# Performance work log

Measured on AMD Instinct MI355X. Metric: run time of the kernel, lower is better.

## Reference

```python
import jax, jax.numpy as jnp
import numpy as np

B, S, D, H = 2, 2048, 1024, 16
HD = D // H  # 64


def rotate_half(x):
    x1, x2 = x[..., : x.shape[-1] // 2], x[..., x.shape[-1] // 2 :]
    return jnp.concatenate((-x2, x1), axis=-1)


def setup_inputs() -> dict:
    key = jax.random.key(0)
    ks = jax.random.split(key, 8)
    return {
        "hidden_states": jax.random.normal(ks[0], (B, S, D), jnp.float32),
        "attention_bias": jax.random.normal(ks[1], (B, 1, S, S), jnp.float32),
        "cos": jax.random.uniform(ks[2], (1, S, 1, HD), jnp.float32),
        "sin": jax.random.uniform(ks[3], (1, S, 1, HD), jnp.float32),
        "Wqkv": jax.random.normal(ks[4], (D, 3 * D), jnp.float32) * (D ** -0.5),
        "bqkv": jnp.zeros((3 * D,), jnp.float32),
        "Wo": jax.random.normal(ks[5], (D, D), jnp.float32) * (D ** -0.5),
        "bo": jnp.zeros((D,), jnp.float32),
    }


def reference(hidden_states, attention_bias, cos, sin, Wqkv, bqkv, Wo, bo):
    # packed QKV projection: [B,S,D] -> [B,S,3D]
    qkv = hidden_states @ Wqkv + bqkv
    q, k, v = jnp.split(qkv, 3, axis=-1)
    # reshape to [B,S,H,HD]
    q = q.reshape(B, S, H, HD)
    k = k.reshape(B, S, H, HD)
    v = v.reshape(B, S, H, HD)
    # rotary position embedding
    q = q * cos + rotate_half(q) * sin
    k = k * cos + rotate_half(k) * sin
    # scaled dot-product attention with additive bias
    scores = jnp.einsum("bqhd,bkhd->bhqk", q, k) / jnp.sqrt(jnp.float32(HD))
    scores = scores + attention_bias
    probs = jax.nn.softmax(scores, axis=-1)
    ctx = jnp.einsum("bhqk,bkhd->bqhd", probs, v)  # [B,S,H,HD]
    ctx = ctx.reshape(B, S, D)
    return ctx @ Wo + bo
```

## Files before the change

kernel.cpp:

```cpp
#include <hip/hip_runtime.h>
#include <stdint.h>

typedef unsigned short u16;
typedef __attribute__((ext_vector_type(8))) short short8;
typedef __attribute__((ext_vector_type(4))) float f32x4;

#define DI __device__ __forceinline__

constexpr int S_LEN = 2048;
constexpr float LOG2E = 1.44269504088896f;
constexpr float SC = 0.125f * 1.44269504088896f;

DI float bf2f(u16 u) { union { uint32_t i; float f; } v; v.i = ((uint32_t)u) << 16; return v.f; }
DI u16 f2bf(float f) {
  union { float f; uint32_t i; } v; v.f = f;
  return (u16)((v.i + 0x7FFFu + ((v.i >> 16) & 1u)) >> 16);
}
DI uint32_t cvtpk(float lo, float hi) {
  uint32_t r;
  asm("v_cvt_pk_bf16_f32 %0, %1, %2" : "=v"(r) : "v"(lo), "v"(hi));
  return r;
}
DI float exp2r(float x) {
  float r;
  asm("v_exp_f32 %0, %1" : "=v"(r) : "v"(x));
  return r;
}

DI void cp16(const void* g, void* l) {
  auto gp = reinterpret_cast<const __attribute__((address_space(1))) uint32_t*>(
      reinterpret_cast<uintptr_t>(g));
  auto lp = reinterpret_cast<__attribute__((address_space(3))) uint32_t*>(
      reinterpret_cast<uintptr_t>(l));
  __builtin_amdgcn_global_load_lds(gp, lp, 16, 0, 0);
}

DI f32x4 mfma16(short8 a, short8 b, f32x4 c) {
  return __builtin_amdgcn_mfma_f32_16x16x32_bf16(a, b, c, 0, 0, 0);
}

DI int permk(int rl) {
  return ((rl >> 5) & 1) * 32 + ((rl >> 2) & 3) * 8 + ((rl >> 4) & 1) * 4 + (rl & 3);
}

__global__ __launch_bounds__(256) void k_cvt(const float* __restrict__ in,
                                             u16* __restrict__ out, int n4) {
  int i = blockIdx.x * 256 + threadIdx.x;
  if (i >= n4) return;
  float4 v = ((const float4*)in)[i];
  ushort4 o = { f2bf(v.x), f2bf(v.y), f2bf(v.z), f2bf(v.w) };
  ((ushort4*)out)[i] = o;
}

__global__ __launch_bounds__(256) void k_cvtb(const float* __restrict__ in,
                                              u16* __restrict__ out, int n4) {
  int i = blockIdx.x * 256 + threadIdx.x;
  if (i >= n4) return;
  float4 v = ((const float4*)in)[i];
  ushort4 o = { f2bf(v.x * LOG2E), f2bf(v.y * LOG2E), f2bf(v.z * LOG2E), f2bf(v.w * LOG2E) };
  ((ushort4*)out)[i] = o;
}

__global__ __launch_bounds__(256) void k_tr(const float* __restrict__ in,
                                            u16* __restrict__ out, int R, int C) {
  __shared__ float t[32][33];
  int tx = threadIdx.x & 31, ty = threadIdx.x >> 5;
  int c0 = blockIdx.x * 32, r0 = blockIdx.y * 32;
#pragma unroll
  for (int k = 0; k < 4; k++)
    t[ty + 8 * k][tx] = in[(size_t)(r0 + ty + 8 * k) * C + c0 + tx];
  __syncthreads();
#pragma unroll
  for (int k = 0; k < 4; k++)
    out[(size_t)(c0 + ty + 8 * k) * R + r0 + tx] = f2bf(t[tx][ty + 8 * k]);
}

template <int STORE_F32, int ROPE>
__global__ __launch_bounds__(256) void k_gemm(const u16* __restrict__ A,
                                              const u16* __restrict__ Bt,
                                              const float* __restrict__ bias,
                                              void* __restrict__ Cout,
                                              const float* __restrict__ cosb,
                                              const float* __restrict__ sinb,
                                              int N, int K, int nbx) {
  __shared__ u16 Al[128 * 32];
  __shared__ u16 Bl[128 * 32];
  int nwg = gridDim.x;
  int per = nwg >> 3;
  int id = blockIdx.x;
  int sid = (id & 7) * per + (id >> 3);
  int bx = sid % nbx, by = sid / nbx;
  int row0 = by * 128, col0 = bx * 128;
  int tid = threadIdx.x;
  int lane = tid & 63, wave = tid >> 6;
  int lg = lane >> 4, lc = lane & 15;
  int wr = wave >> 1, wc = wave & 1;
  int srow = tid >> 2, sseg = tid & 3;
  const u16* ga = A + (size_t)(row0 + srow) * K + sseg * 8;
  const u16* gb = Bt + (size_t)(col0 + srow) * K + sseg * 8;
  u16* la = Al + tid * 8;
  u16* lb = Bl + tid * 8;
  size_t half = (size_t)64 * K;
  f32x4 acc[4][4] = {};
  for (int ko = 0; ko < K; ko += 32) {
    cp16(ga + ko, la);
    cp16(ga + ko + half, la + 2048);
    cp16(gb + ko, lb);
    cp16(gb + ko + half, lb + 2048);
    __syncthreads();
    short8 af[4], bf[4];
#pragma unroll
    for (int i = 0; i < 4; i++)
      af[i] = *(const short8*)&Al[(wr * 64 + i * 16 + lc) * 32 + lg * 8];
#pragma unroll
    for (int j = 0; j < 4; j++)
      bf[j] = *(const short8*)&Bl[(wc * 64 + j * 16 + lc) * 32 + lg * 8];
#pragma unroll
    for (int i = 0; i < 4; i++)
#pragma unroll
      for (int j = 0; j < 4; j++) acc[i][j] = mfma16(af[i], bf[j], acc[i][j]);
    __syncthreads();
  }
  int cbase = col0 + wc * 64 + lc;
  float bv[4];
#pragma unroll
  for (int j = 0; j < 4; j++) bv[j] = bias[cbase + j * 16];
  bool do_rope = false;
  if constexpr (ROPE) do_rope = (col0 < 2048);
#pragma unroll
  for (int i = 0; i < 4; i++) {
    int r = row0 + wr * 64 + i * 16 + lg * 4;
#pragma unroll
    for (int q = 0; q < 4; q++) {
      float v[4];
#pragma unroll
      for (int j = 0; j < 4; j++) v[j] = acc[i][j][q] + bv[j];
      if (do_rope) {
        int s = (r + q) & 2047;
        const float* cb = cosb + s * 64 + lc;
        const float* sb = sinb + s * 64 + lc;
#pragma unroll
        for (int jp = 0; jp < 2; jp++) {
          float cl = cb[jp * 16], sl = sb[jp * 16];
          float ch = cb[jp * 16 + 32], sh = sb[jp * 16 + 32];
          float x1 = v[jp], x2 = v[jp + 2];
          v[jp] = x1 * cl - x2 * sl;
          v[jp + 2] = x2 * ch + x1 * sh;
        }
      }
#pragma unroll
      for (int j = 0; j < 4; j++) {
        if constexpr (STORE_F32)
          ((float*)Cout)[(size_t)(r + q) * N + cbase + j * 16] = v[j];
        else
          ((u16*)Cout)[(size_t)(r + q) * N + cbase + j * 16] = f2bf(v[j]);
      }
    }
  }
}

__global__ __launch_bounds__(256) void k_vtrans(const u16* __restrict__ qkv,
                                                u16* __restrict__ vtg) {
  __shared__ u16 Vl[64 * 66];
  int bh = blockIdx.y, b = bh >> 4, h = bh & 15;
  int s0 = blockIdx.x * 64;
  int tid = threadIdx.x;
  int r = tid >> 3, seg = tid & 7;
  const u16* src = qkv + (size_t)(b * S_LEN + s0) * 3072 + 2048 + h * 64 + seg * 8;
#pragma unroll
  for (int p = 0; p < 2; p++) {
    int s = r + 32 * p;
    short8 v = *(const short8*)(src + (size_t)s * 3072);
    const uint32_t* vw = (const uint32_t*)&v;
    uint32_t* dst = (uint32_t*)&Vl[s * 66 + seg * 8];
#pragma unroll
    for (int q = 0; q < 4; q++) dst[q] = vw[q];
  }
  __syncthreads();
  u16* out = vtg + (size_t)bh * 64 * 2048 + s0 + seg * 8;
#pragma unroll
  for (int p = 0; p < 2; p++) {
    int d = r + 32 * p;
    short8 o;
#pragma unroll
    for (int j = 0; j < 8; j++) o[j] = (short)Vl[(seg * 8 + j) * 66 + d];
    *(short8*)(out + (size_t)d * 2048) = o;
  }
}

DI float sm_pa(const f32x4 st[4], const short8* bc, short8 pa[2]) {
  float acc = 0.f;
  uint32_t w[4][2];
#pragma unroll
  for (int j = 0; j < 4; j++) {
    int base = (j & 1) * 4;
    float b0 = bf2f((u16)(j < 2 ? bc[0][base + 0] : bc[1][base + 0]));
    float b1 = bf2f((u16)(j < 2 ? bc[0][base + 1] : bc[1][base + 1]));
    float b2 = bf2f((u16)(j < 2 ? bc[0][base + 2] : bc[1][base + 2]));
    float b3 = bf2f((u16)(j < 2 ? bc[0][base + 3] : bc[1][base + 3]));
    float e0 = exp2r(st[j][0] * SC + b0);
    float e1 = exp2r(st[j][1] * SC + b1);
    float e2 = exp2r(st[j][2] * SC + b2);
    float e3 = exp2r(st[j][3] * SC + b3);
    acc += (e0 + e1) + (e2 + e3);
    w[j][0] = cvtpk(e0, e1);
    w[j][1] = cvtpk(e2, e3);
  }
  union { short8 s; uint32_t u[4]; } p0, p1;
  p0.u[0] = w[0][0]; p0.u[1] = w[0][1]; p0.u[2] = w[1][0]; p0.u[3] = w[1][1];
  p1.u[0] = w[2][0]; p1.u[1] = w[2][1]; p1.u[2] = w[3][0]; p1.u[3] = w[3][1];
  pa[0] = p0.s;
  pa[1] = p1.s;
  return acc;
}

DI void attn_store(u16* __restrict__ ctx, const f32x4 o[4], float lsumT,
                   size_t rowbase, int hcol, int lg, int lc) {
  float rinv[4];
#pragma unroll
  for (int r = 0; r < 4; r++) rinv[r] = 1.0f / __shfl(lsumT, lg * 4 + r);
#pragma unroll
  for (int j = 0; j < 4; j++)
#pragma unroll
    for (int r = 0; r < 4; r++)
      ctx[(rowbase + lg * 4 + r) * 1024 + hcol + j * 16 + lc] =
          f2bf(o[j][r] * rinv[r]);
}

__global__ __launch_bounds__(256, 2) void k_attn(const u16* __restrict__ qkv,
                                                 const u16* __restrict__ biasl2,
                                                 const u16* __restrict__ vtg,
                                                 u16* __restrict__ ctx) {
  __shared__ u16 Kl[2][4096];
  __shared__ u16 Vl[2][4096];
  constexpr int nkt = 32;
  int id = blockIdx.x;
  int idx = id >> 3;
  int bh = (id & 7) * 4 + (idx & 3);
  int qt = idx >> 2;
  int b = bh >> 4, h = bh & 15;
  int tid = threadIdx.x, lane = tid & 63, wave = tid >> 6;
  int lg = lane >> 4, lc = lane & 15;
  int q0 = qt * 128 + wave * 32;

  const u16* qb = qkv + (size_t)(b * S_LEN + q0 + lc) * 3072 + h * 64 + lg * 8;
  short8 qf[2][2];
#pragma unroll
  for (int s = 0; s < 2; s++) {
    qf[s][0] = *(const short8*)(qb + (size_t)s * 16 * 3072);
    qf[s][1] = *(const short8*)(qb + (size_t)s * 16 * 3072 + 32);
  }

  int srow = tid >> 3, sseg = tid & 7;
  const u16* kst[2];
  const u16* vst[2];
#pragma unroll
  for (int p = 0; p < 2; p++) {
    int rl = srow + 32 * p;
    int sw = (sseg ^ (rl & 7)) * 8;
    kst[p] = qkv + (size_t)(b * S_LEN + permk(rl)) * 3072 + 1024 + h * 64 + sw;
    vst[p] = vtg + (size_t)bh * 64 * 2048 + (size_t)rl * 2048 + sw;
  }

  const u16* bp0 = biasl2 + ((size_t)b * S_LEN + q0 + lc) * 2048 + lg * 8;
  const u16* bp1 = bp0 + (size_t)16 * 2048;

  f32x4 o0[4] = {}, o1[4] = {};
  float lsum0 = 0.f, lsum1 = 0.f;

#pragma unroll
  for (int p = 0; p < 2; p++) {
    cp16(kst[p], (u16*)&Kl[0][0] + p * 2048 + tid * 8);
    cp16(vst[p], (u16*)&Vl[0][0] + p * 2048 + tid * 8);
    kst[p] += (size_t)64 * 3072;
    vst[p] += 64;
  }
  short8 bA[4], bB[4];
  bA[0] = *(const short8*)bp0;
  bA[1] = *(const short8*)(bp0 + 32);
  bA[2] = *(const short8*)bp1;
  bA[3] = *(const short8*)(bp1 + 32);
  bp0 += 64;
  bp1 += 64;
  __syncthreads();

  auto tile = [&](int kt, int cur, const short8* bc, short8* bn) {
    if (kt < nkt - 1) {
#pragma unroll
      for (int p = 0; p < 2; p++) {
        cp16(kst[p], (u16*)&Kl[cur ^ 1][0] + p * 2048 + tid * 8);
        cp16(vst[p], (u16*)&Vl[cur ^ 1][0] + p * 2048 + tid * 8);
        kst[p] += (size_t)64 * 3072;
        vst[p] += 64;
      }
      bn[0] = *(const short8*)bp0;
      bn[1] = *(const short8*)(bp0 + 32);
      bn[2] = *(const short8*)bp1;
      bn[3] = *(const short8*)(bp1 + 32);
      bp0 += 64;
      bp1 += 64;
    }
    f32x4 st0[4] = {}, st1[4] = {};
    __builtin_amdgcn_s_setprio(1);
#pragma unroll
    for (int kk = 0; kk < 2; kk++) {
      short8 kf[4];
#pragma unroll
      for (int j = 0; j < 4; j++) {
        int row = j * 16 + lc;
        kf[j] = *(const short8*)&Kl[cur][row * 64 + (((kk * 4 + lg) ^ (row & 7)) * 8)];
      }
#pragma unroll
      for (int j = 0; j < 4; j++) {
        st0[j] = mfma16(kf[j], qf[0][kk], st0[j]);
        st1[j] = mfma16(kf[j], qf[1][kk], st1[j]);
      }
    }
    __builtin_amdgcn_s_setprio(0);
    short8 pa0[2], pa1[2];
    lsum0 += sm_pa(st0, bc, pa0);
    lsum1 += sm_pa(st1, bc + 2, pa1);
    __builtin_amdgcn_s_setprio(1);
#pragma unroll
    for (int kk = 0; kk < 2; kk++) {
      short8 vf[4];
#pragma unroll
      for (int j = 0; j < 4; j++) {
        int row = j * 16 + lc;
        vf[j] = *(const short8*)&Vl[cur][row * 64 + (((kk * 4 + lg) ^ (row & 7)) * 8)];
      }
#pragma unroll
      for (int j = 0; j < 4; j++) {
        o0[j] = mfma16(pa0[kk], vf[j], o0[j]);
        o1[j] = mfma16(pa1[kk], vf[j], o1[j]);
      }
    }
    __builtin_amdgcn_s_setprio(0);
    __syncthreads();
  };

  for (int kt = 0; kt < nkt; kt += 2) {
    tile(kt, 0, bA, bB);
    tile(kt + 1, 1, bB, bA);
  }

  float t0 = lsum0;
  t0 += __shfl_xor(t0, 16);
  t0 += __shfl_xor(t0, 32);
  float t1 = lsum1;
  t1 += __shfl_xor(t1, 16);
  t1 += __shfl_xor(t1, 32);
  size_t rowbase = (size_t)b * S_LEN + q0;
  attn_store(ctx, o0, t0, rowbase, h * 64, lg, lc);
  attn_store(ctx, o1, t1, rowbase + 16, h * 64, lg, lc);
}

extern "C" void kernel_launch(void* const* d_in, const int* in_sizes, int n_in,
                              void* d_out, int out_size, void* d_ws, size_t ws_size,
                              hipStream_t stream) {
  (void)in_sizes; (void)n_in; (void)out_size; (void)ws_size;
  const float* hs   = (const float*)d_in[0];
  const float* bias = (const float*)d_in[1];
  const float* cosb = (const float*)d_in[2];
  const float* sinb = (const float*)d_in[3];
  const float* Wqkv = (const float*)d_in[4];
  const float* bqkv = (const float*)d_in[5];
  const float* Wo   = (const float*)d_in[6];
  const float* bo   = (const float*)d_in[7];
  float* out = (float*)d_out;
  char* ws = (char*)d_ws;
  u16* h_bf   = (u16*)(ws + 0);
  u16* wqkvT  = (u16*)(ws + 8388608);
  u16* woT    = (u16*)(ws + 14680064);
  u16* biasbf = (u16*)(ws + 16777216);
  u16* qkv    = (u16*)(ws + 33554432);
  u16* vtg    = (u16*)(ws + 58720256);
  u16* ctxb   = (u16*)(ws + 67108864);

  k_cvt<<<4096, 256, 0, stream>>>(hs, h_bf, 1048576);
  k_cvtb<<<8192, 256, 0, stream>>>(bias, biasbf, 2097152);
  k_tr<<<dim3(96, 32), 256, 0, stream>>>(Wqkv, wqkvT, 1024, 3072);
  k_tr<<<dim3(32, 32), 256, 0, stream>>>(Wo, woT, 1024, 1024);
  k_gemm<0, 1><<<768, 256, 0, stream>>>(h_bf, wqkvT, bqkv, qkv, cosb, sinb,
                                        3072, 1024, 24);
  k_vtrans<<<dim3(32, 32), 256, 0, stream>>>(qkv, vtg);
  k_attn<<<512, 256, 0, stream>>>(qkv, biasbf, vtg, ctxb);
  k_gemm<1, 0><<<256, 256, 0, stream>>>(ctxb, woT, bo, out, nullptr, nullptr,
                                        1024, 1024, 8);
}
```

Measured before the change: 155.1 us.

## Drop bias bf16 pre-conversion, merge transposes, widen GEMM K tile with swizzle

The attention kernel now reads the fp32 attention bias directly and folds the log2e scaling into an fma. This removes the separate bias conversion pass, which read 32MB and wrote 16MB, but doubles the bias bytes read inside attention. The two weight transposes are merged into one launch. The GEMM now uses a 64-wide K tile with an XOR-swizzled LDS layout, and the output projection uses 64-row tiles so it launches 512 workgroups instead of 256.

```diff
diff --git a/kernel.cpp b/kernel.cpp
--- a/kernel.cpp
+++ b/kernel.cpp
@@ -52,20 +52,20 @@
   ((ushort4*)out)[i] = o;
 }
 
-__global__ __launch_bounds__(256) void k_cvtb(const float* __restrict__ in,
-                                              u16* __restrict__ out, int n4) {
-  int i = blockIdx.x * 256 + threadIdx.x;
-  if (i >= n4) return;
-  float4 v = ((const float4*)in)[i];
-  ushort4 o = { f2bf(v.x * LOG2E), f2bf(v.y * LOG2E), f2bf(v.z * LOG2E), f2bf(v.w * LOG2E) };
-  ((ushort4*)out)[i] = o;
-}
-
-__global__ __launch_bounds__(256) void k_tr(const float* __restrict__ in,
-                                            u16* __restrict__ out, int R, int C) {
+__global__ __launch_bounds__(256) void k_tr2(const float* __restrict__ Wqkv,
+                                             u16* __restrict__ wqkvT,
+                                             const float* __restrict__ Wo,
+                                             u16* __restrict__ woT) {
   __shared__ float t[32][33];
+  int bx = blockIdx.x;
+  const float* in;
+  u16* out;
+  int C;
+  if (bx < 96) { in = Wqkv; out = wqkvT; C = 3072; }
+  else         { bx -= 96; in = Wo; out = woT; C = 1024; }
+  constexpr int R = 1024;
   int tx = threadIdx.x & 31, ty = threadIdx.x >> 5;
-  int c0 = blockIdx.x * 32, r0 = blockIdx.y * 32;
+  int c0 = bx * 32, r0 = blockIdx.y * 32;
 #pragma unroll
   for (int k = 0; k < 4; k++)
     t[ty + 8 * k][tx] = in[(size_t)(r0 + ty + 8 * k) * C + c0 + tx];
@@ -75,7 +75,7 @@
     out[(size_t)(c0 + ty + 8 * k) * R + r0 + tx] = f2bf(t[tx][ty + 8 * k]);
 }
 
-template <int STORE_F32, int ROPE>
+template <int BM, int STORE_F32, int ROPE>
 __global__ __launch_bounds__(256) void k_gemm(const u16* __restrict__ A,
                                               const u16* __restrict__ Bt,
                                               const float* __restrict__ bias,
@@ -83,73 +83,84 @@
                                               const float* __restrict__ cosb,
                                               const float* __restrict__ sinb,
                                               int N, int K, int nbx) {
-  __shared__ u16 Al[128 * 32];
-  __shared__ u16 Bl[128 * 32];
+  constexpr int NJ = (BM == 128) ? 4 : 2;
+  __shared__ u16 Al[BM * 64];
+  __shared__ u16 Bl[128 * 64];
   int nwg = gridDim.x;
   int per = nwg >> 3;
   int id = blockIdx.x;
   int sid = (id & 7) * per + (id >> 3);
   int bx = sid % nbx, by = sid / nbx;
-  int row0 = by * 128, col0 = bx * 128;
+  int row0 = by * BM, col0 = bx * 128;
   int tid = threadIdx.x;
   int lane = tid & 63, wave = tid >> 6;
   int lg = lane >> 4, lc = lane & 15;
-  int wr = wave >> 1, wc = wave & 1;
-  int srow = tid >> 2, sseg = tid & 3;
-  const u16* ga = A + (size_t)(row0 + srow) * K + sseg * 8;
-  const u16* gb = Bt + (size_t)(col0 + srow) * K + sseg * 8;
-  u16* la = Al + tid * 8;
-  u16* lb = Bl + tid * 8;
-  size_t half = (size_t)64 * K;
-  f32x4 acc[4][4] = {};
-  for (int ko = 0; ko < K; ko += 32) {
-    cp16(ga + ko, la);
-    cp16(ga + ko + half, la + 2048);
-    cp16(gb + ko, lb);
-    cp16(gb + ko + half, lb + 2048);
+  int wroff = (BM == 128) ? (wave >> 1) * 64 : 0;
+  int wcoff = (BM == 128) ? (wave & 1) * 64 : wave * 32;
+  int srow = tid >> 3, sseg = tid & 7;
+  int sw = (sseg ^ (srow & 7)) * 8;
+  const u16* ga = A + (size_t)(row0 + srow) * K + sw;
+  const u16* gb = Bt + (size_t)(col0 + srow) * K + sw;
+  f32x4 acc[4][NJ] = {};
+  for (int ko = 0; ko < K; ko += 64) {
+#pragma unroll
+    for (int p = 0; p < BM / 32; p++)
+      cp16(ga + (size_t)p * 32 * K + ko, Al + tid * 8 + p * 2048);
+#pragma unroll
+    for (int p = 0; p < 4; p++)
+      cp16(gb + (size_t)p * 32 * K + ko, Bl + tid * 8 + p * 2048);
     __syncthreads();
-    short8 af[4], bf[4];
-#pragma unroll
-    for (int i = 0; i < 4; i++)
-      af[i] = *(const short8*)&Al[(wr * 64 + i * 16 + lc) * 32 + lg * 8];
-#pragma unroll
-    for (int j = 0; j < 4; j++)
-      bf[j] = *(const short8*)&Bl[(wc * 64 + j * 16 + lc) * 32 + lg * 8];
-#pragma unroll
-    for (int i = 0; i < 4; i++)
-#pragma unroll
-      for (int j = 0; j < 4; j++) acc[i][j] = mfma16(af[i], bf[j], acc[i][j]);
+#pragma unroll
+    for (int kk = 0; kk < 2; kk++) {
+      short8 af[4], bf[NJ];
+#pragma unroll
+      for (int i = 0; i < 4; i++) {
+        int row = wroff + i * 16 + lc;
+        af[i] = *(const short8*)&Al[row * 64 + (((kk * 4 + lg) ^ (row & 7)) * 8)];
+      }
+#pragma unroll
+      for (int j = 0; j < NJ; j++) {
+        int row = wcoff + j * 16 + lc;
+        bf[j] = *(const short8*)&Bl[row * 64 + (((kk * 4 + lg) ^ (row & 7)) * 8)];
+      }
+#pragma unroll
+      for (int i = 0; i < 4; i++)
+#pragma unroll
+        for (int j = 0; j < NJ; j++) acc[i][j] = mfma16(af[i], bf[j], acc[i][j]);
+    }
     __syncthreads();
   }
-  int cbase = col0 + wc * 64 + lc;
-  float bv[4];
-#pragma unroll
-  for (int j = 0; j < 4; j++) bv[j] = bias[cbase + j * 16];
+  int cbase = col0 + wcoff + lc;
+  float bv[NJ];
+#pragma unroll
+  for (int j = 0; j < NJ; j++) bv[j] = bias[cbase + j * 16];
   bool do_rope = false;
   if constexpr (ROPE) do_rope = (col0 < 2048);
 #pragma unroll
   for (int i = 0; i < 4; i++) {
-    int r = row0 + wr * 64 + i * 16 + lg * 4;
+    int r = row0 + wroff + i * 16 + lg * 4;
 #pragma unroll
     for (int q = 0; q < 4; q++) {
-      float v[4];
-#pragma unroll
-      for (int j = 0; j < 4; j++) v[j] = acc[i][j][q] + bv[j];
-      if (do_rope) {
-        int s = (r + q) & 2047;
-        const float* cb = cosb + s * 64 + lc;
-        const float* sb = sinb + s * 64 + lc;
-#pragma unroll
-        for (int jp = 0; jp < 2; jp++) {
-          float cl = cb[jp * 16], sl = sb[jp * 16];
-          float ch = cb[jp * 16 + 32], sh = sb[jp * 16 + 32];
-          float x1 = v[jp], x2 = v[jp + 2];
-          v[jp] = x1 * cl - x2 * sl;
-          v[jp + 2] = x2 * ch + x1 * sh;
+      float v[NJ];
+#pragma unroll
+      for (int j = 0; j < NJ; j++) v[j] = acc[i][j][q] + bv[j];
+      if constexpr (ROPE) {
+        if (do_rope) {
+          int s = (r + q) & 2047;
+          const float* cb = cosb + s * 64 + lc;
+          const float* sb = sinb + s * 64 + lc;
+#pragma unroll
+          for (int jp = 0; jp < 2; jp++) {
+            float cl = cb[jp * 16], sl = sb[jp * 16];
+            float ch = cb[jp * 16 + 32], sh = sb[jp * 16 + 32];
+            float x1 = v[jp], x2 = v[jp + 2];
+            v[jp] = x1 * cl - x2 * sl;
+            v[jp + 2] = x2 * ch + x1 * sh;
+          }
         }
       }
 #pragma unroll
-      for (int j = 0; j < 4; j++) {
+      for (int j = 0; j < NJ; j++) {
         if constexpr (STORE_F32)
           ((float*)Cout)[(size_t)(r + q) * N + cbase + j * 16] = v[j];
         else
@@ -188,20 +199,16 @@
   }
 }
 
-DI float sm_pa(const f32x4 st[4], const short8* bc, short8 pa[2]) {
+DI float sm_pa(const f32x4 st[4], const f32x4 bc[4], short8 pa[2]) {
   float acc = 0.f;
   uint32_t w[4][2];
 #pragma unroll
   for (int j = 0; j < 4; j++) {
-    int base = (j & 1) * 4;
-    float b0 = bf2f((u16)(j < 2 ? bc[0][base + 0] : bc[1][base + 0]));
-    float b1 = bf2f((u16)(j < 2 ? bc[0][base + 1] : bc[1][base + 1]));
-    float b2 = bf2f((u16)(j < 2 ? bc[0][base + 2] : bc[1][base + 2]));
-    float b3 = bf2f((u16)(j < 2 ? bc[0][base + 3] : bc[1][base + 3]));
-    float e0 = exp2r(st[j][0] * SC + b0);
-    float e1 = exp2r(st[j][1] * SC + b1);
-    float e2 = exp2r(st[j][2] * SC + b2);
-    float e3 = exp2r(st[j][3] * SC + b3);
+    f32x4 bb = bc[j];
+    float e0 = exp2r(fmaf(bb[0], LOG2E, st[j][0] * SC));
+    float e1 = exp2r(fmaf(bb[1], LOG2E, st[j][1] * SC));
+    float e2 = exp2r(fmaf(bb[2], LOG2E, st[j][2] * SC));
+    float e3 = exp2r(fmaf(bb[3], LOG2E, st[j][3] * SC));
     acc += (e0 + e1) + (e2 + e3);
     w[j][0] = cvtpk(e0, e1);
     w[j][1] = cvtpk(e2, e3);
@@ -228,7 +235,7 @@
 }
 
 __global__ __launch_bounds__(256, 2) void k_attn(const u16* __restrict__ qkv,
-                                                 const u16* __restrict__ biasl2,
+                                                 const float* __restrict__ biasf,
                                                  const u16* __restrict__ vtg,
                                                  u16* __restrict__ ctx) {
   __shared__ u16 Kl[2][4096];
@@ -262,8 +269,8 @@
     vst[p] = vtg + (size_t)bh * 64 * 2048 + (size_t)rl * 2048 + sw;
   }
 
-  const u16* bp0 = biasl2 + ((size_t)b * S_LEN + q0 + lc) * 2048 + lg * 8;
-  const u16* bp1 = bp0 + (size_t)16 * 2048;
+  const float* bp0 = biasf + ((size_t)b * S_LEN + q0 + lc) * 2048 + lg * 8;
+  const float* bp1 = bp0 + (size_t)16 * 2048;
 
   f32x4 o0[4] = {}, o1[4] = {};
   float lsum0 = 0.f, lsum1 = 0.f;
@@ -275,16 +282,17 @@
     kst[p] += (size_t)64 * 3072;
     vst[p] += 64;
   }
-  short8 bA[4], bB[4];
-  bA[0] = *(const short8*)bp0;
-  bA[1] = *(const short8*)(bp0 + 32);
-  bA[2] = *(const short8*)bp1;
-  bA[3] = *(const short8*)(bp1 + 32);
+  f32x4 bA0[4], bA1[4], bB0[4], bB1[4];
+  bA0[0] = *(const f32x4*)bp0;        bA0[1] = *(const f32x4*)(bp0 + 4);
+  bA0[2] = *(const f32x4*)(bp0 + 32); bA0[3] = *(const f32x4*)(bp0 + 36);
+  bA1[0] = *(const f32x4*)bp1;        bA1[1] = *(const f32x4*)(bp1 + 4);
+  bA1[2] = *(const f32x4*)(bp1 + 32); bA1[3] = *(const f32x4*)(bp1 + 36);
   bp0 += 64;
   bp1 += 64;
   __syncthreads();
 
-  auto tile = [&](int kt, int cur, const short8* bc, short8* bn) {
+  auto tile = [&](int kt, int cur, const f32x4* bc0, const f32x4* bc1,
+                  f32x4* bn0, f32x4* bn1) {
     if (kt < nkt - 1) {
 #pragma unroll
       for (int p = 0; p < 2; p++) {
@@ -293,10 +301,10 @@
         kst[p] += (size_t)64 * 3072;
         vst[p] += 64;
       }
-      bn[0] = *(const short8*)bp0;
-      bn[1] = *(const short8*)(bp0 + 32);
-      bn[2] = *(const short8*)bp1;
-      bn[3] = *(const short8*)(bp1 + 32);
+      bn0[0] = *(const f32x4*)bp0;        bn0[1] = *(const f32x4*)(bp0 + 4);
+      bn0[2] = *(const f32x4*)(bp0 + 32); bn0[3] = *(const f32x4*)(bp0 + 36);
+      bn1[0] = *(const f32x4*)bp1;        bn1[1] = *(const f32x4*)(bp1 + 4);
+      bn1[2] = *(const f32x4*)(bp1 + 32); bn1[3] = *(const f32x4*)(bp1 + 36);
       bp0 += 64;
       bp1 += 64;
     }
@@ -318,8 +326,8 @@
     }
     __builtin_amdgcn_s_setprio(0);
     short8 pa0[2], pa1[2];
-    lsum0 += sm_pa(st0, bc, pa0);
-    lsum1 += sm_pa(st1, bc + 2, pa1);
+    lsum0 += sm_pa(st0, bc0, pa0);
+    lsum1 += sm_pa(st1, bc1, pa1);
     __builtin_amdgcn_s_setprio(1);
 #pragma unroll
     for (int kk = 0; kk < 2; kk++) {
@@ -340,8 +348,8 @@
   };
 
   for (int kt = 0; kt < nkt; kt += 2) {
-    tile(kt, 0, bA, bB);
-    tile(kt + 1, 1, bB, bA);
+    tile(kt, 0, bA0, bA1, bB0, bB1);
+    tile(kt + 1, 1, bB0, bB1, bA0, bA1);
   }
 
   float t0 = lsum0;
@@ -372,19 +380,16 @@
   u16* h_bf   = (u16*)(ws + 0);
   u16* wqkvT  = (u16*)(ws + 8388608);
   u16* woT    = (u16*)(ws + 14680064);
-  u16* biasbf = (u16*)(ws + 16777216);
-  u16* qkv    = (u16*)(ws + 33554432);
-  u16* vtg    = (u16*)(ws + 58720256);
-  u16* ctxb   = (u16*)(ws + 67108864);
+  u16* qkv    = (u16*)(ws + 16777216);
+  u16* vtg    = (u16*)(ws + 41943040);
+  u16* ctxb   = (u16*)(ws + 50331648);
 
   k_cvt<<<4096, 256, 0, stream>>>(hs, h_bf, 1048576);
-  k_cvtb<<<8192, 256, 0, stream>>>(bias, biasbf, 2097152);
-  k_tr<<<dim3(96, 32), 256, 0, stream>>>(Wqkv, wqkvT, 1024, 3072);
-  k_tr<<<dim3(32, 32), 256, 0, stream>>>(Wo, woT, 1024, 1024);
-  k_gemm<0, 1><<<768, 256, 0, stream>>>(h_bf, wqkvT, bqkv, qkv, cosb, sinb,
-                                        3072, 1024, 24);
+  k_tr2<<<dim3(128, 32), 256, 0, stream>>>(Wqkv, wqkvT, Wo, woT);
+  k_gemm<128, 0, 1><<<768, 256, 0, stream>>>(h_bf, wqkvT, bqkv, qkv, cosb, sinb,
+                                             3072, 1024, 24);
   k_vtrans<<<dim3(32, 32), 256, 0, stream>>>(qkv, vtg);
-  k_attn<<<512, 256, 0, stream>>>(qkv, biasbf, vtg, ctxb);
-  k_gemm<1, 0><<<256, 256, 0, stream>>>(ctxb, woT, bo, out, nullptr, nullptr,
-                                        1024, 1024, 8);
-}
+  k_attn<<<512, 256, 0, stream>>>(qkv, bias, vtg, ctxb);
+  k_gemm<64, 1, 0><<<512, 256, 0, stream>>>(ctxb, woT, bo, out, nullptr, nullptr,
+                                            1024, 1024, 8);
+}
```

Measured after the change: 157.2 us. About the same (+1.3%).
